# Optimization experiments

Hardware: AMD Instinct MI355X
Metric: run time of the kernel (lower is better)

Reference implementation:

```python
import jax, jax.numpy as jnp
import numpy as np

B, C, H, W_ = 4, 3, 224, 224
K = 196          # max_segments
E = 768          # embed_dim


def setup_inputs() -> dict:
    key = jax.random.key(0)
    k1, k2, k3 = jax.random.split(key, 3)
    img = jax.random.normal(k1, (B, C, H, W_), dtype=jnp.float32)
    segments = jax.random.randint(k2, (B, H, W_), 0, K, dtype=jnp.int32)
    W = jax.random.normal(k3, (C, E), dtype=jnp.float32) * 0.02
    b = jnp.zeros((E,), dtype=jnp.float32)
    return {"img": img, "segments": segments, "W": W, "b": b}


def reference(img, segments, W, b):
    # Per-segment one-hot masked bucketing (the torch loop, vectorized):
    # segment_features[b,k,c,h,w] = img[b,c,h,w] * (segments[b,h,w] == k)
    onehot = jax.nn.one_hot(segments, K, dtype=img.dtype)           # (B,H,W,K)
    seg_feat = jnp.einsum('bhwk,bchw->bkchw', onehot, img)          # (B,K,C,H,W)
    # Feature extractor stand-in: spatial mean pool + linear C->E
    pooled = seg_feat.mean(axis=(3, 4))                              # (B,K,C)
    out = jnp.einsum('bkc,ce->bke', pooled, W) + b                   # (B,K,E)
    return out
```

## Files before the change

kernel.cpp:

```cpp
#include <hip/hip_runtime.h>

#define Bn  4
#define Cn  3
#define Hn  224
#define Wn  224
#define Kn  196
#define En  768
#define HW  (Hn * Wn)
#define BPB 49
#define NPOOL (Bn * BPB)
#define KC  (Kn * Cn)

__global__ __launch_bounds__(256) void seg_pool_partial(
    const float* __restrict__ img,
    const int*   __restrict__ seg,
    float*       __restrict__ partials)
{
    __shared__ float acc[KC];
    const int tid = threadIdx.x;
    for (int i = tid; i < KC; i += 256) acc[i] = 0.0f;
    __syncthreads();

    const int batch = blockIdx.x / BPB;
    const int blk   = blockIdx.x % BPB;
    const int p4    = blk * 256 + tid;

    const int4*   seg4 = (const int4*)(seg + (size_t)batch * HW);
    const float4* im   = (const float4*)(img + (size_t)batch * Cn * HW);

    const int4   s  = seg4[p4];
    const float4 v0 = im[p4];
    const float4 v1 = im[HW / 4 + p4];
    const float4 v2 = im[2 * (HW / 4) + p4];

    atomicAdd(&acc[s.x * 3 + 0], v0.x);
    atomicAdd(&acc[s.x * 3 + 1], v1.x);
    atomicAdd(&acc[s.x * 3 + 2], v2.x);
    atomicAdd(&acc[s.y * 3 + 0], v0.y);
    atomicAdd(&acc[s.y * 3 + 1], v1.y);
    atomicAdd(&acc[s.y * 3 + 2], v2.y);
    atomicAdd(&acc[s.z * 3 + 0], v0.z);
    atomicAdd(&acc[s.z * 3 + 1], v1.z);
    atomicAdd(&acc[s.z * 3 + 2], v2.z);
    atomicAdd(&acc[s.w * 3 + 0], v0.w);
    atomicAdd(&acc[s.w * 3 + 1], v1.w);
    atomicAdd(&acc[s.w * 3 + 2], v2.w);
    __syncthreads();

    float4* dst = (float4*)(partials + (size_t)blockIdx.x * KC);
    if (tid < KC / 4) dst[tid] = ((const float4*)acc)[tid];
}

__global__ __launch_bounds__(192) void embed_kernel(
    const float* __restrict__ partials,
    const float* __restrict__ Wm,
    const float* __restrict__ bias,
    float*       __restrict__ out)
{
    __shared__ float part[BPB * 3];
    __shared__ float sums[3];
    const int b   = blockIdx.x / Kn;
    const int k   = blockIdx.x % Kn;
    const int tid = threadIdx.x;

    if (tid < BPB * 3) {
        const int j = tid / 3;
        const int c = tid % 3;
        part[tid] = partials[(size_t)(b * BPB + j) * KC + k * 3 + c];
    }
    __syncthreads();

    if (tid < 3) {
        float s = 0.0f;
        #pragma unroll
        for (int j = 0; j < BPB; ++j) s += part[j * 3 + tid];
        sums[tid] = s * (1.0f / (float)HW);
    }
    __syncthreads();

    const float p0 = sums[0];
    const float p1 = sums[1];
    const float p2 = sums[2];

    const float4 w0 = ((const float4*)(Wm          ))[tid];
    const float4 w1 = ((const float4*)(Wm +     En ))[tid];
    const float4 w2 = ((const float4*)(Wm + 2 * En ))[tid];
    const float4 bb = ((const float4*)bias)[tid];

    float4 r;
    r.x = p0 * w0.x + p1 * w1.x + p2 * w2.x + bb.x;
    r.y = p0 * w0.y + p1 * w1.y + p2 * w2.y + bb.y;
    r.z = p0 * w0.z + p1 * w1.z + p2 * w2.z + bb.z;
    r.w = p0 * w0.w + p1 * w1.w + p2 * w2.w + bb.w;
    ((float4*)out)[(size_t)blockIdx.x * (En / 4) + tid] = r;
}

extern "C" void kernel_launch(void* const* d_in, const int* in_sizes, int n_in,
                              void* d_out, int out_size, void* d_ws, size_t ws_size,
                              hipStream_t stream) {
    const float* img  = (const float*)d_in[0];
    const int*   seg  = (const int*)  d_in[1];
    const float* Wm   = (const float*)d_in[2];
    const float* bias = (const float*)d_in[3];
    float* out      = (float*)d_out;
    float* partials = (float*)d_ws;

    seg_pool_partial<<<NPOOL, 256, 0, stream>>>(img, seg, partials);
    embed_kernel<<<Bn * Kn, 192, 0, stream>>>(partials, Wm, bias, out);
}
```

Baseline: 67.82 us.

## Transpose partials layout, privatize LDS histograms, and use wave-level reduction in embed

The pooling kernel now keeps two shared-memory histograms, one per half of the block, to reduce atomic contention. It writes partial sums transposed so each (segment, channel) row holds its block partials contiguously. The embed kernel reduces a row with wavefront shuffles instead of LDS plus serial loops, and handles four segments per 256-thread block. The trade-off is strided scattered writes in the first kernel in exchange for coalesced reads and fewer syncs in the second.

```diff
diff --git a/kernel.cpp b/kernel.cpp
--- a/kernel.cpp
+++ b/kernel.cpp
@@ -14,16 +14,17 @@
 __global__ __launch_bounds__(256) void seg_pool_partial(
     const float* __restrict__ img,
     const int*   __restrict__ seg,
-    float*       __restrict__ partials)
+    float*       __restrict__ partialsT)
 {
-    __shared__ float acc[KC];
+    __shared__ float acc[2][KC];
     const int tid = threadIdx.x;
-    for (int i = tid; i < KC; i += 256) acc[i] = 0.0f;
+    for (int i = tid; i < 2 * KC; i += 256) ((float*)acc)[i] = 0.0f;
     __syncthreads();
 
     const int batch = blockIdx.x / BPB;
     const int blk   = blockIdx.x % BPB;
     const int p4    = blk * 256 + tid;
+    const int h     = tid >> 7;
 
     const int4*   seg4 = (const int4*)(seg + (size_t)batch * HW);
     const float4* im   = (const float4*)(img + (size_t)batch * Cn * HW);
@@ -33,66 +34,71 @@
     const float4 v1 = im[HW / 4 + p4];
     const float4 v2 = im[2 * (HW / 4) + p4];
 
-    atomicAdd(&acc[s.x * 3 + 0], v0.x);
-    atomicAdd(&acc[s.x * 3 + 1], v1.x);
-    atomicAdd(&acc[s.x * 3 + 2], v2.x);
-    atomicAdd(&acc[s.y * 3 + 0], v0.y);
-    atomicAdd(&acc[s.y * 3 + 1], v1.y);
-    atomicAdd(&acc[s.y * 3 + 2], v2.y);
-    atomicAdd(&acc[s.z * 3 + 0], v0.z);
-    atomicAdd(&acc[s.z * 3 + 1], v1.z);
-    atomicAdd(&acc[s.z * 3 + 2], v2.z);
-    atomicAdd(&acc[s.w * 3 + 0], v0.w);
-    atomicAdd(&acc[s.w * 3 + 1], v1.w);
-    atomicAdd(&acc[s.w * 3 + 2], v2.w);
+    float* a = acc[h];
+    atomicAdd(&a[s.x * 3 + 0], v0.x);
+    atomicAdd(&a[s.x * 3 + 1], v1.x);
+    atomicAdd(&a[s.x * 3 + 2], v2.x);
+    atomicAdd(&a[s.y * 3 + 0], v0.y);
+    atomicAdd(&a[s.y * 3 + 1], v1.y);
+    atomicAdd(&a[s.y * 3 + 2], v2.y);
+    atomicAdd(&a[s.z * 3 + 0], v0.z);
+    atomicAdd(&a[s.z * 3 + 1], v1.z);
+    atomicAdd(&a[s.z * 3 + 2], v2.z);
+    atomicAdd(&a[s.w * 3 + 0], v0.w);
+    atomicAdd(&a[s.w * 3 + 1], v1.w);
+    atomicAdd(&a[s.w * 3 + 2], v2.w);
     __syncthreads();
 
-    float4* dst = (float4*)(partials + (size_t)blockIdx.x * KC);
-    if (tid < KC / 4) dst[tid] = ((const float4*)acc)[tid];
+    float* dst = partialsT + (size_t)batch * KC * BPB + blk;
+    for (int sidx = tid; sidx < KC; sidx += 256)
+        dst[(size_t)sidx * BPB] = acc[0][sidx] + acc[1][sidx];
 }
 
-__global__ __launch_bounds__(192) void embed_kernel(
-    const float* __restrict__ partials,
+__global__ __launch_bounds__(256) void embed_kernel(
+    const float* __restrict__ partialsT,
     const float* __restrict__ Wm,
     const float* __restrict__ bias,
     float*       __restrict__ out)
 {
-    __shared__ float part[BPB * 3];
-    __shared__ float sums[3];
-    const int b   = blockIdx.x / Kn;
-    const int k   = blockIdx.x % Kn;
-    const int tid = threadIdx.x;
+    const int tid  = threadIdx.x;
+    const int lane = tid & 63;
+    const int wv   = tid >> 6;
+    const int b    = blockIdx.x / BPB;
+    const int k    = (blockIdx.x % BPB) * 4 + wv;
 
-    if (tid < BPB * 3) {
-        const int j = tid / 3;
-        const int c = tid % 3;
-        part[tid] = partials[(size_t)(b * BPB + j) * KC + k * 3 + c];
+    const float* row = partialsT + ((size_t)b * KC + k * 3) * BPB;
+    float a0 = (lane < BPB) ? row[lane]           : 0.0f;
+    float a1 = (lane < BPB) ? row[BPB + lane]     : 0.0f;
+    float a2 = (lane < BPB) ? row[2 * BPB + lane] : 0.0f;
+
+    #pragma unroll
+    for (int off = 32; off > 0; off >>= 1) {
+        a0 += __shfl_xor(a0, off, 64);
+        a1 += __shfl_xor(a1, off, 64);
+        a2 += __shfl_xor(a2, off, 64);
     }
-    __syncthreads();
+    const float p0 = a0 * (1.0f / (float)HW);
+    const float p1 = a1 * (1.0f / (float)HW);
+    const float p2 = a2 * (1.0f / (float)HW);
 
-    if (tid < 3) {
-        float s = 0.0f;
-        #pragma unroll
-        for (int j = 0; j < BPB; ++j) s += part[j * 3 + tid];
-        sums[tid] = s * (1.0f / (float)HW);
+    const float4* W4 = (const float4*)Wm;
+    const float4* B4 = (const float4*)bias;
+    float4* O4 = (float4*)out + ((size_t)b * Kn + k) * (En / 4);
+
+    #pragma unroll
+    for (int part = 0; part < 3; ++part) {
+        const int idx = part * 64 + lane;
+        const float4 w0 = W4[idx];
+        const float4 w1 = W4[192 + idx];
+        const float4 w2 = W4[384 + idx];
+        const float4 bb = B4[idx];
+        float4 r;
+        r.x = p0 * w0.x + p1 * w1.x + p2 * w2.x + bb.x;
+        r.y = p0 * w0.y + p1 * w1.y + p2 * w2.y + bb.y;
+        r.z = p0 * w0.z + p1 * w1.z + p2 * w2.z + bb.z;
+        r.w = p0 * w0.w + p1 * w1.w + p2 * w2.w + bb.w;
+        O4[idx] = r;
     }
-    __syncthreads();
-
-    const float p0 = sums[0];
-    const float p1 = sums[1];
-    const float p2 = sums[2];
-
-    const float4 w0 = ((const float4*)(Wm          ))[tid];
-    const float4 w1 = ((const float4*)(Wm +     En ))[tid];
-    const float4 w2 = ((const float4*)(Wm + 2 * En ))[tid];
-    const float4 bb = ((const float4*)bias)[tid];
-
-    float4 r;
-    r.x = p0 * w0.x + p1 * w1.x + p2 * w2.x + bb.x;
-    r.y = p0 * w0.y + p1 * w1.y + p2 * w2.y + bb.y;
-    r.z = p0 * w0.z + p1 * w1.z + p2 * w2.z + bb.z;
-    r.w = p0 * w0.w + p1 * w1.w + p2 * w2.w + bb.w;
-    ((float4*)out)[(size_t)blockIdx.x * (En / 4) + tid] = r;
 }
 
 extern "C" void kernel_launch(void* const* d_in, const int* in_sizes, int n_in,
@@ -102,9 +108,9 @@
     const int*   seg  = (const int*)  d_in[1];
     const float* Wm   = (const float*)d_in[2];
     const float* bias = (const float*)d_in[3];
-    float* out      = (float*)d_out;
-    float* partials = (float*)d_ws;
+    float* out       = (float*)d_out;
+    float* partialsT = (float*)d_ws;
 
-    seg_pool_partial<<<NPOOL, 256, 0, stream>>>(img, seg, partials);
-    embed_kernel<<<Bn * Kn, 192, 0, stream>>>(partials, Wm, bias, out);
+    seg_pool_partial<<<NPOOL, 256, 0, stream>>>(img, seg, partialsT);
+    embed_kernel<<<NPOOL, 256, 0, stream>>>(partialsT, Wm, bias, out);
 }
```

Result: no change. 67.00 us (-1.2%).
